# Kernel optimization log

Measured on AMD Instinct MI355X. Metric: run time of the kernel, lower is better.

Reference implementation:

```python
import jax, jax.numpy as jnp
import numpy as np

NUM_HEADS = 16
MEMORY_LR = 0.1


def setup_inputs() -> dict:
    key = jax.random.key(0)
    ks = jax.random.split(key, 5)
    B, S, D = 4, 4096, 1024
    x = jax.random.normal(ks[0], (B, S, D), dtype=jnp.float32)
    # torch init: randn * 0.01, shape (out_features, in_features)
    Wq = jax.random.normal(ks[1], (D, D), dtype=jnp.float32) * 0.01
    Wk = jax.random.normal(ks[2], (D, D), dtype=jnp.float32) * 0.01
    Wv = jax.random.normal(ks[3], (D, D), dtype=jnp.float32) * 0.01
    Wo = jax.random.normal(ks[4], (D, D), dtype=jnp.float32) * 0.01
    return {"x": x, "Wq": Wq, "Wk": Wk, "Wv": Wv, "Wo": Wo}


def reference(x, Wq, Wk, Wv, Wo):
    B, S, D = x.shape
    H = NUM_HEADS
    hd = D // H
    # Projections (torch Linear: y = x @ W^T). Pending self-mod updates
    # (immediate_update=False) never change W during forward -> plain matmul.
    Q = (x @ Wq.T).reshape(B, S, H, hd)
    K = (x @ Wk.T).reshape(B, S, H, hd)
    V = (x @ Wv.T).reshape(B, S, H, hd)
    # time-major for scan: [S, B, H, hd]
    Qt = jnp.transpose(Q, (1, 0, 2, 3))
    Kt = jnp.transpose(K, (1, 0, 2, 3))
    Vt = jnp.transpose(V, (1, 0, 2, 3))

    def step(M, qkv):
        q, k, v = qkv  # each [B, H, hd]
        v_pred = jnp.einsum('hdk,bhk->bhd', M, k)
        err = v - v_pred
        # torch computes the update under no_grad -> constant w.r.t. params
        upd = jax.lax.stop_gradient(jnp.einsum('bhd,bhk->hdk', err, k) / B)
        M_new = M + MEMORY_LR * upd
        out = jnp.einsum('hdk,bhk->bhd', M_new, q)
        return M_new, out

    M0 = jnp.zeros((H, hd, hd), dtype=x.dtype)  # memory buffer starts at zero
    _, outs = jax.lax.scan(step, M0, (Qt, Kt, Vt))  # outs: [S, B, H, hd]
    out = jnp.transpose(outs, (1, 0, 2, 3)).reshape(B, S, D)
    # dropout p=0.0 -> identity
    return out @ Wo.T
```

## Files before the change

### kernel.cpp

```cpp
#include <hip/hip_runtime.h>


typedef unsigned short u16;
typedef __attribute__((ext_vector_type(8))) short short8;
typedef __attribute__((ext_vector_type(4))) float f32x4;

#define B_ 4
#define S_ 4096
#define D_ 1024
#define H_ 16
#define CHUNK 16
#define NCHUNK 256
#define SUPW 16
#define NSUP 16
#define ETA 0.025f

__device__ __forceinline__ u16 f2bf(float f) {
  unsigned u = __builtin_bit_cast(unsigned, f);
  u += 0x7fffu + ((u >> 16) & 1u);
  return (u16)(u >> 16);
}
__device__ __forceinline__ float bf2f(u16 s) {
  unsigned u = ((unsigned)s) << 16;
  return __builtin_bit_cast(float, u);
}
__device__ __forceinline__ float ldv(float v) { return v; }
__device__ __forceinline__ float ldv(u16 v) { return bf2f(v); }
__device__ __forceinline__ void stv(float* p, float v) { *p = v; }
__device__ __forceinline__ void stv(u16* p, float v) { *p = f2bf(v); }

#define MFMA __builtin_amdgcn_mfma_f32_16x16x32_bf16

__device__ __forceinline__ void gload16(const void* g, void* l) {
  __builtin_amdgcn_global_load_lds(
      (__attribute__((address_space(1))) void*)g,
      (__attribute__((address_space(3))) void*)l, 16, 0, 0);
}

__global__ void cvt_hi_kernel(const float* __restrict__ x, u16* __restrict__ hi, int n4) {
  int i = blockIdx.x * blockDim.x + threadIdx.x;
  int stride = gridDim.x * blockDim.x;
  for (; i < n4; i += stride) {
    float4 v = ((const float4*)x)[i];
    ushort4 h;
    h.x = f2bf(v.x); h.y = f2bf(v.y); h.z = f2bf(v.z); h.w = f2bf(v.w);
    ((ushort4*)hi)[i] = h;
  }
}

template<int BPRE, typename OutT>
__global__ __launch_bounds__(256) void gemm_axw(
    const u16* __restrict__ Ahg, const void* __restrict__ Bhp,
    OutT* __restrict__ C, int M, int N, int K) {
  __shared__ __align__(16) u16 Ahs[2][128][32];
  __shared__ __align__(16) u16 Bhs[2][128][32];
  const int tid = threadIdx.x, w = tid >> 6, lane = tid & 63;
  const int nwg = gridDim.x * gridDim.y;
  const int orig = blockIdx.y * gridDim.x + blockIdx.x;
  const int id = ((nwg & 7) == 0) ? ((orig & 7) * (nwg >> 3) + (orig >> 3)) : orig;
  const int bm = (id % gridDim.x) * 128, bn = (id / gridDim.x) * 128;
  const int wm = (w >> 1) * 64, wn = (w & 1) * 64;
  const int fr = lane & 15, kb = lane >> 4;
  const int lrow = lane >> 2, lcol = (lane & 3) * 8;

  auto stage = [&](int buf, int k0) {
    {
      const size_t rb = (size_t)(bm + w * 32 + lrow) * K + k0 + lcol;
      gload16(Ahg + rb, &Ahs[buf][w * 32][0]);
      gload16(Ahg + rb + (size_t)16 * K, &Ahs[buf][w * 32 + 16][0]);
    }
    if constexpr (BPRE) {
      const u16* Bhg = (const u16*)Bhp;
      const size_t rb = (size_t)(bn + w * 32 + lrow) * K + k0 + lcol;
      gload16(Bhg + rb, &Bhs[buf][w * 32][0]);
      gload16(Bhg + rb + (size_t)16 * K, &Bhs[buf][w * 32 + 16][0]);
    } else {
      const float* Bm = (const float*)Bhp;
#pragma unroll
      for (int i2 = 0; i2 < 4; ++i2) {
        int e = tid + i2 * 256, r = e >> 3, sg = (e & 7) * 4;
        float4 v = *(const float4*)(&Bm[(size_t)(bn + r) * K + k0 + sg]);
        ushort4 hq;
        hq.x = f2bf(v.x); hq.y = f2bf(v.y); hq.z = f2bf(v.z); hq.w = f2bf(v.w);
        *(ushort4*)(&Bhs[buf][r][sg]) = hq;
      }
    }
  };

  f32x4 acc[4][4];
#pragma unroll
  for (int i = 0; i < 4; ++i)
#pragma unroll
    for (int j = 0; j < 4; ++j) acc[i][j] = (f32x4){0.f, 0.f, 0.f, 0.f};

  stage(0, 0);
  asm volatile("s_waitcnt vmcnt(0)" ::: "memory");
  __syncthreads();
  const int nt = K >> 5;
  int cur = 0;
  for (int t = 0; t < nt; ++t) {
    if (t + 1 < nt) stage(cur ^ 1, (t + 1) * 32);
    short8 ah[4], bh[4];
#pragma unroll
    for (int mi = 0; mi < 4; ++mi)
      ah[mi] = *(const short8*)(&Ahs[cur][wm + mi * 16 + fr][kb * 8]);
#pragma unroll
    for (int ni = 0; ni < 4; ++ni)
      bh[ni] = *(const short8*)(&Bhs[cur][wn + ni * 16 + fr][kb * 8]);
#pragma unroll
    for (int mi = 0; mi < 4; ++mi)
#pragma unroll
      for (int ni = 0; ni < 4; ++ni)
        acc[mi][ni] = MFMA(ah[mi], bh[ni], acc[mi][ni], 0, 0, 0);
    asm volatile("s_waitcnt vmcnt(0)" ::: "memory");
    __syncthreads();
    cur ^= 1;
  }
  const int fc = lane & 15, fr4 = (lane >> 4) * 4;
#pragma unroll
  for (int mi = 0; mi < 4; ++mi)
#pragma unroll
    for (int ni = 0; ni < 4; ++ni) {
      int gm = bm + wm + mi * 16 + fr4;
      int gn = bn + wn + ni * 16 + fc;
#pragma unroll
      for (int rg = 0; rg < 4; ++rg)
        stv(&C[(size_t)(gm + rg) * N + gn], acc[mi][ni][rg]);
    }
}

template<typename PT>
__global__ __launch_bounds__(256) void phase1_kernel(
    float* __restrict__ Qg, const u16* __restrict__ Kg, u16* __restrict__ Vg,
    PT* __restrict__ Pg, PT* __restrict__ Rg) {
  __shared__ __align__(16) u16 Ks[64][72];
  __shared__ __align__(16) u16 KsT[64][72];
  __shared__ __align__(16) u16 Gh[64][72];
  __shared__ __align__(16) u16 Gl[64][72];
  __shared__ __align__(16) float Ut[64][68];
  __shared__ __align__(16) float Wt[64][68];

  const int c = blockIdx.x, h = blockIdx.y, tid = threadIdx.x;
  const int w = tid >> 6, lane = tid & 63;
  const int fr = lane & 15, kq = lane >> 4, orow = kq * 4;
  const int xr = 16 * w + fr;

  auto gidx = [&](int r, int d) -> size_t {
    return ((size_t)(r & 3) * S_ + (size_t)c * CHUNK + (r >> 2)) * D_ + h * 64 + d;
  };
  auto ldb = [&](const u16 (*M)[72], int row, int s) -> short8 {
    return *(const short8*)(&M[row][32 * s + 8 * kq]);
  };
  auto ldm = [&](const u16 (*M)[72], int row, int s, bool up) -> short8 {
    short8 r = *(const short8*)(&M[row][32 * s + 8 * kq]);
    int rb = row >> 2, k0 = 32 * s + 8 * kq;
#pragma unroll
    for (int j = 0; j < 8; ++j) {
      int kb2 = (k0 + j) >> 2;
      bool keep = up ? (kb2 > rb) : (rb > kb2);
      if (!keep) r[j] = 0;
    }
    return r;
  };
  auto ldf = [&](const float (*M)[68], int row, int s, short8& hh, short8& ll) {
    const float* p = &M[row][32 * s + 8 * kq];
#pragma unroll
    for (int j = 0; j < 8; ++j) {
      float v = p[j];
      u16 hb = f2bf(v);
      hh[j] = (short)hb;
      ll[j] = (short)f2bf(v - bf2f(hb));
    }
  };
  auto ldfh = [&](const float (*M)[68], int row, int s) -> short8 {
    const float* p = &M[row][32 * s + 8 * kq];
    short8 hh;
#pragma unroll
    for (int j = 0; j < 8; ++j) hh[j] = (short)f2bf(p[j]);
    return hh;
  };

  for (int i = tid; i < 4096; i += 256) {
    int r = i >> 6, d = i & 63;
    size_t g = gidx(r, d);
    u16 kraw = Kg[g];
    Ks[r][d] = kraw;
    KsT[d][r] = kraw;
    Wt[d][r] = ETA * bf2f(kraw);
    Ut[d][r] = ETA * bf2f(Vg[g]);
  }
  __syncthreads();

  {
    f32x4 acc[4];
#pragma unroll
    for (int ni = 0; ni < 4; ++ni) acc[ni] = (f32x4){0.f, 0.f, 0.f, 0.f};
    short8 xf[2];
#pragma unroll
    for (int s = 0; s < 2; ++s) xf[s] = ldb(Ks, xr, s);
#pragma unroll
    for (int ni = 0; ni < 4; ++ni)
#pragma unroll
      for (int s = 0; s < 2; ++s)
        acc[ni] = MFMA(xf[s], ldb(Ks, 16 * ni + fr, s), acc[ni], 0, 0, 0);
#pragma unroll
    for (int ni = 0; ni < 4; ++ni)
#pragma unroll
      for (int rg = 0; rg < 4; ++rg) {
        float v = -ETA * acc[ni][rg];
        u16 hb = f2bf(v);
        int rr = 16 * w + orow + rg, cc = 16 * ni + fr;
        Gh[rr][cc] = hb;
        Gl[rr][cc] = f2bf(v - bf2f(hb));
      }
  }

  float sreg[4][4];
  {
    short8 xh[2], xl[2];
#pragma unroll
    for (int s = 0; s < 2; ++s) {
      const float* qp = &Qg[gidx(xr, 32 * s + 8 * kq)];
#pragma unroll
      for (int j = 0; j < 8; ++j) {
        float v = qp[j];
        u16 hb = f2bf(v);
        xh[s][j] = (short)hb;
        xl[s][j] = (short)f2bf(v - bf2f(hb));
      }
    }
    f32x4 acc[4];
#pragma unroll
    for (int ni = 0; ni < 4; ++ni) acc[ni] = (f32x4){0.f, 0.f, 0.f, 0.f};
#pragma unroll
    for (int ni = 0; ni < 4; ++ni)
#pragma unroll
      for (int s = 0; s < 2; ++s) {
        short8 yf = ldb(Ks, 16 * ni + fr, s);
        acc[ni] = MFMA(xh[s], yf, acc[ni], 0, 0, 0);
        acc[ni] = MFMA(xl[s], yf, acc[ni], 0, 0, 0);
      }
#pragma unroll
    for (int ni = 0; ni < 4; ++ni)
#pragma unroll
      for (int rg = 0; rg < 4; ++rg) {
        int r = 16 * w + orow + rg, cc = 16 * ni + fr;
        sreg[ni][rg] = ((r >> 2) >= (cc >> 2)) ? acc[ni][rg] : 0.f;
      }
  }
  __syncthreads();

  auto app1 = [&](float (*St)[68]) {
    short8 xh[2], xl[2];
#pragma unroll
    for (int s = 0; s < 2; ++s) ldf(St, xr, s, xh[s], xl[s]);
    f32x4 acc[4];
#pragma unroll
    for (int ni = 0; ni < 4; ++ni) acc[ni] = (f32x4){0.f, 0.f, 0.f, 0.f};
#pragma unroll
    for (int ni = 0; ni < 4; ++ni)
#pragma unroll
      for (int s = 0; s < 2; ++s) {
        short8 yh = ldm(Gh, 16 * ni + fr, s, false);
        short8 yl = ldm(Gl, 16 * ni + fr, s, false);
        acc[ni] = MFMA(xh[s], yh, acc[ni], 0, 0, 0);
        acc[ni] = MFMA(xh[s], yl, acc[ni], 0, 0, 0);
        acc[ni] = MFMA(xl[s], yh, acc[ni], 0, 0, 0);
      }
#pragma unroll
    for (int ni = 0; ni < 4; ++ni)
#pragma unroll
      for (int rg = 0; rg < 4; ++rg)
        St[16 * w + orow + rg][16 * ni + fr] += acc[ni][rg];
  };
  auto appS = [&](float (*St)[68], const u16 (*Np)[72]) {
    short8 xh[2];
#pragma unroll
    for (int s = 0; s < 2; ++s) xh[s] = ldfh(St, xr, s);
    f32x4 acc[4];
#pragma unroll
    for (int ni = 0; ni < 4; ++ni) acc[ni] = (f32x4){0.f, 0.f, 0.f, 0.f};
#pragma unroll
    for (int ni = 0; ni < 4; ++ni)
#pragma unroll
      for (int s = 0; s < 2; ++s)
        acc[ni] = MFMA(xh[s], ldb(Np, 16 * ni + fr, s), acc[ni], 0, 0, 0);
#pragma unroll
    for (int ni = 0; ni < 4; ++ni)
#pragma unroll
      for (int rg = 0; rg < 4; ++rg)
        St[16 * w + orow + rg][16 * ni + fr] += acc[ni][rg];
  };

  app1(Ut);
  app1(Wt);
  {
    f32x4 sq[4];
#pragma unroll
    for (int ni = 0; ni < 4; ++ni) sq[ni] = (f32x4){0.f, 0.f, 0.f, 0.f};
    short8 xh[2], xl[2];
#pragma unroll
    for (int s = 0; s < 2; ++s) {
      xh[s] = ldm(Gh, xr, s, false);
      xl[s] = ldm(Gl, xr, s, false);
    }
#pragma unroll
    for (int ni = 0; ni < 4; ++ni)
#pragma unroll
      for (int s = 0; s < 2; ++s) {
        short8 yh = ldm(Gh, 16 * ni + fr, s, true);
        short8 yl = ldm(Gl, 16 * ni + fr, s, true);
        sq[ni] = MFMA(xh[s], yh, sq[ni], 0, 0, 0);
        sq[ni] = MFMA(xh[s], yl, sq[ni], 0, 0, 0);
        sq[ni] = MFMA(xl[s], yh, sq[ni], 0, 0, 0);
      }
    __syncthreads();
#pragma unroll
    for (int ni = 0; ni < 4; ++ni)
#pragma unroll
      for (int rg = 0; rg < 4; ++rg) {
        u16 b = f2bf(sq[ni][rg]);
        int rr = 16 * w + orow + rg, cc = 16 * ni + fr;
        Ks[rr][cc] = b;
        Gh[cc][rr] = b;
      }
  }
  __syncthreads();

  appS(Ut, Ks);
  appS(Wt, Ks);
  {
    f32x4 sq[4];
#pragma unroll
    for (int ni = 0; ni < 4; ++ni) sq[ni] = (f32x4){0.f, 0.f, 0.f, 0.f};
    short8 xf[2];
#pragma unroll
    for (int s = 0; s < 2; ++s) xf[s] = ldb(Ks, xr, s);
#pragma unroll
    for (int ni = 0; ni < 4; ++ni)
#pragma unroll
      for (int s = 0; s < 2; ++s)
        sq[ni] = MFMA(xf[s], ldb(Gh, 16 * ni + fr, s), sq[ni], 0, 0, 0);
    __syncthreads();
#pragma unroll
    for (int ni = 0; ni < 4; ++ni)
#pragma unroll
      for (int rg = 0; rg < 4; ++rg) {
        u16 b = f2bf(sq[ni][rg]);
        int rr = 16 * w + orow + rg, cc = 16 * ni + fr;
        Gl[rr][cc] = b;
        Ks[cc][rr] = b;
      }
  }
  __syncthreads();

  appS(Ut, Gl);
  appS(Wt, Gl);
  {
    f32x4 sq[4];
#pragma unroll
    for (int ni = 0; ni < 4; ++ni) sq[ni] = (f32x4){0.f, 0.f, 0.f, 0.f};
    short8 xf[2];
#pragma unroll
    for (int s = 0; s < 2; ++s) xf[s] = ldb(Gl, xr, s);
#pragma unroll
    for (int ni = 0; ni < 4; ++ni)
#pragma unroll
      for (int s = 0; s < 2; ++s)
        sq[ni] = MFMA(xf[s], ldb(Ks, 16 * ni + fr, s), sq[ni], 0, 0, 0);
#pragma unroll
    for (int ni = 0; ni < 4; ++ni)
#pragma unroll
      for (int rg = 0; rg < 4; ++rg)
        Gh[16 * w + orow + rg][16 * ni + fr] = f2bf(sq[ni][rg]);
  }
  __syncthreads();

  appS(Ut, Gh);
  appS(Wt, Gh);
  __syncthreads();

  const size_t base = ((size_t)c * H_ + h) * 4096;
  {
    short8 xh[2], xl[2];
#pragma unroll
    for (int s = 0; s < 2; ++s) ldf(Wt, xr, s, xh[s], xl[s]);
    f32x4 acc[4];
#pragma unroll
    for (int ni = 0; ni < 4; ++ni) acc[ni] = (f32x4){0.f, 0.f, 0.f, 0.f};
#pragma unroll
    for (int ni = 0; ni < 4; ++ni)
#pragma unroll
      for (int s = 0; s < 2; ++s) {
        short8 yf = ldb(KsT, 16 * ni + fr, s);
        acc[ni] = MFMA(xh[s], yf, acc[ni], 0, 0, 0);
        acc[ni] = MFMA(xl[s], yf, acc[ni], 0, 0, 0);
      }
#pragma unroll
    for (int ni = 0; ni < 4; ++ni)
#pragma unroll
      for (int rg = 0; rg < 4; ++rg)
        stv(&Pg[base + (16 * w + orow + rg) * 64 + 16 * ni + fr], acc[ni][rg]);
  }
  {
    short8 xh[2], xl[2];
#pragma unroll
    for (int s = 0; s < 2; ++s) ldf(Ut, xr, s, xh[s], xl[s]);
    f32x4 acc[4];
#pragma unroll
    for (int ni = 0; ni < 4; ++ni) acc[ni] = (f32x4){0.f, 0.f, 0.f, 0.f};
#pragma unroll
    for (int ni = 0; ni < 4; ++ni)
#pragma unroll
      for (int s = 0; s < 2; ++s) {
        short8 yf = ldb(KsT, 16 * ni + fr, s);
        acc[ni] = MFMA(xh[s], yf, acc[ni], 0, 0, 0);
        acc[ni] = MFMA(xl[s], yf, acc[ni], 0, 0, 0);
      }
#pragma unroll
    for (int ni = 0; ni < 4; ++ni)
#pragma unroll
      for (int rg = 0; rg < 4; ++rg)
        stv(&Rg[base + (16 * w + orow + rg) * 64 + 16 * ni + fr], acc[ni][rg]);
  }
  {
    const int r = tid >> 2, d0 = (tid & 3) * 16;
    short8 v0, v1;
#pragma unroll
    for (int j = 0; j < 8; ++j) v0[j] = (short)f2bf(Wt[r][d0 + j]);
#pragma unroll
    for (int j = 0; j < 8; ++j) v1[j] = (short)f2bf(Wt[r][d0 + 8 + j]);
    *(short8*)(&Gh[r][d0]) = v0;
    *(short8*)(&Gh[r][d0 + 8]) = v1;
#pragma unroll
    for (int j = 0; j < 8; ++j) v0[j] = (short)f2bf(Ut[r][d0 + j]);
#pragma unroll
    for (int j = 0; j < 8; ++j) v1[j] = (short)f2bf(Ut[r][d0 + 8 + j]);
    *(short8*)(&Gl[r][d0]) = v0;
    *(short8*)(&Gl[r][d0 + 8]) = v1;
  }
#pragma unroll
  for (int ni = 0; ni < 4; ++ni)
#pragma unroll
    for (int rg = 0; rg < 4; ++rg)
      Ks[16 * w + orow + rg][16 * ni + fr] = f2bf(sreg[ni][rg]);
  __syncthreads();

  {
    short8 xs[2];
#pragma unroll
    for (int s = 0; s < 2; ++s) xs[s] = ldb(Ks, xr, s);
    f32x4 accE[4], accF[4];
#pragma unroll
    for (int ni = 0; ni < 4; ++ni) {
      accE[ni] = (f32x4){0.f, 0.f, 0.f, 0.f};
      accF[ni] = (f32x4){0.f, 0.f, 0.f, 0.f};
    }
#pragma unroll
    for (int ni = 0; ni < 4; ++ni)
#pragma unroll
      for (int s = 0; s < 2; ++s) {
        accE[ni] = MFMA(xs[s], ldb(Gh, 16 * ni + fr, s), accE[ni], 0, 0, 0);
        accF[ni] = MFMA(xs[s], ldb(Gl, 16 * ni + fr, s), accF[ni], 0, 0, 0);
      }
#pragma unroll
    for (int ni = 0; ni < 4; ++ni)
#pragma unroll
      for (int rg = 0; rg < 4; ++rg) {
        int r = 16 * w + orow + rg, d = 16 * ni + fr;
        size_t g = gidx(r, d);
        float qv = Qg[g];
        Qg[g] = qv - accE[ni][rg];
        Vg[g] = f2bf(accF[ni][rg]);
      }
  }
}

__device__ __forceinline__ void store64(float* dst, const float (*src)[65], int tid) {
  for (int i = tid; i < 4096; i += 256) dst[i] = src[i >> 6][i & 63];
}
__device__ __forceinline__ void mm64(const float (*X)[65], const float (*Y)[65],
                                     float (*Dst)[65], const float (*Add)[65], int tid) {
  const int r0 = (tid >> 4) * 4, c0 = (tid & 15) * 4;
  float a[4][4] = {};
  for (int d = 0; d < 64; ++d) {
    float xv[4], yv[4];
#pragma unroll
    for (int i = 0; i < 4; ++i) xv[i] = X[r0 + i][d];
#pragma unroll
    for (int j = 0; j < 4; ++j) yv[j] = Y[d][c0 + j];
#pragma unroll
    for (int i = 0; i < 4; ++i)
#pragma unroll
      for (int j = 0; j < 4; ++j) a[i][j] += xv[i] * yv[j];
  }
  __syncthreads();
#pragma unroll
  for (int i = 0; i < 4; ++i)
#pragma unroll
    for (int j = 0; j < 4; ++j) {
      float v = a[i][j];
      if (Add) v += Add[r0 + i][c0 + j];
      Dst[r0 + i][c0 + j] = v;
    }
  __syncthreads();
}

template<typename PT>
__global__ __launch_bounds__(256) void seq_levelA(const PT* __restrict__ Pg,
    const PT* __restrict__ Rg, float* __restrict__ Psup, float* __restrict__ Rsup) {
  __shared__ __align__(16) float Pa[64][68], Ra[64][68], Ri[64][68];
  __shared__ __align__(16) u16 Pih[64][72], Pil[64][72];
  const int sup = blockIdx.x, h = blockIdx.y, tid = threadIdx.x;
  const int w = tid >> 6, lane = tid & 63;
  const int fr = lane & 15, kq = lane >> 4, orow = kq * 4;
  const int xr = 16 * w + fr;
  const int cbase = sup * SUPW;

  auto upd = [&](float (*St)[68], const float (*Add)[68]) {
    short8 xh[2], xl[2];
#pragma unroll
    for (int s2 = 0; s2 < 2; ++s2) {
      const float* p = &St[xr][32 * s2 + 8 * kq];
#pragma unroll
      for (int j = 0; j < 8; ++j) {
        float v = p[j];
        u16 hb = f2bf(v);
        xh[s2][j] = (short)hb;
        xl[s2][j] = (short)f2bf(v - bf2f(hb));
      }
    }
    f32x4 acc[4];
#pragma unroll
    for (int ni = 0; ni < 4; ++ni) acc[ni] = (f32x4){0.f, 0.f, 0.f, 0.f};
#pragma unroll
    for (int ni = 0; ni < 4; ++ni)
#pragma unroll
      for (int s2 = 0; s2 < 2; ++s2) {
        short8 yh = *(const short8*)(&Pih[16 * ni + fr][32 * s2 + 8 * kq]);
        short8 yl = *(const short8*)(&Pil[16 * ni + fr][32 * s2 + 8 * kq]);
        acc[ni] = MFMA(xh[s2], yh, acc[ni], 0, 0, 0);
        acc[ni] = MFMA(xh[s2], yl, acc[ni], 0, 0, 0);
        acc[ni] = MFMA(xl[s2], yh, acc[ni], 0, 0, 0);
      }
#pragma unroll
    for (int ni = 0; ni < 4; ++ni)
#pragma unroll
      for (int rg = 0; rg < 4; ++rg) {
        float v = acc[ni][rg];
        if (Add) v += Add[16 * w + orow + rg][16 * ni + fr];
        St[16 * w + orow + rg][16 * ni + fr] = v;
      }
  };

  {
    const PT* ps = Pg + ((size_t)cbase * H_ + h) * 4096;
    const PT* rs = Rg + ((size_t)cbase * H_ + h) * 4096;
    for (int i = tid; i < 4096; i += 256) {
      int r = i >> 6, cc = i & 63;
      Pa[r][cc] = ((r == cc) ? 1.f : 0.f) - ldv(ps[i]);
      Ra[r][cc] = ldv(rs[i]);
    }
  }
  float pf[16], rf[16];
  {
    const PT* ps = Pg + ((size_t)(cbase + 1) * H_ + h) * 4096;
    const PT* rs = Rg + ((size_t)(cbase + 1) * H_ + h) * 4096;
#pragma unroll
    for (int k = 0; k < 16; ++k) { int i = tid + k * 256; pf[k] = ldv(ps[i]); rf[k] = ldv(rs[i]); }
  }
  for (int s = 1; s < SUPW; ++s) {
#pragma unroll
    for (int k = 0; k < 16; ++k) {
      int i = tid + k * 256, d = i >> 6, cc = i & 63;
      float v = ((d == cc) ? 1.f : 0.f) - pf[k];
      u16 hb = f2bf(v);
      Pih[cc][d] = hb;
      Pil[cc][d] = f2bf(v - bf2f(hb));
      Ri[d][cc] = rf[k];
    }
    __syncthreads();
    if (s + 1 < SUPW) {
      const PT* ps = Pg + ((size_t)(cbase + s + 1) * H_ + h) * 4096;
      const PT* rs = Rg + ((size_t)(cbase + s + 1) * H_ + h) * 4096;
#pragma unroll
      for (int k = 0; k < 16; ++k) { int i = tid + k * 256; pf[k] = ldv(ps[i]); rf[k] = ldv(rs[i]); }
    }
    upd(Pa, nullptr);
    upd(Ra, Ri);
    __syncthreads();
  }
  for (int i = tid; i < 4096; i += 256) {
    Psup[((size_t)sup * H_ + h) * 4096 + i] = Pa[i >> 6][i & 63];
    Rsup[((size_t)sup * H_ + h) * 4096 + i] = Ra[i >> 6][i & 63];
  }
}

__global__ __launch_bounds__(256) void seq_levelB(const float* __restrict__ Psup,
    const float* __restrict__ Rsup, float* __restrict__ Msup) {
  __shared__ float Ms[64][65], Pi[64][65], Ri[64][65];
  const int h = blockIdx.x, tid = threadIdx.x;
  for (int i = tid; i < 4096; i += 256) Ms[i >> 6][i & 63] = 0.f;
  float pf[16], rf[16];
  {
    const float* ps = Psup + ((size_t)0 * H_ + h) * 4096;
    const float* rs = Rsup + ((size_t)0 * H_ + h) * 4096;
#pragma unroll
    for (int k = 0; k < 16; ++k) { int i = tid + k * 256; pf[k] = ps[i]; rf[k] = rs[i]; }
  }
  for (int s = 0; s < NSUP; ++s) {
#pragma unroll
    for (int k = 0; k < 16; ++k) {
      int i = tid + k * 256, r = i >> 6, cc = i & 63;
      Pi[r][cc] = pf[k];
      Ri[r][cc] = rf[k];
    }
    store64(Msup + ((size_t)s * H_ + h) * 4096, Ms, tid);
    __syncthreads();
    if (s + 1 < NSUP) {
      const float* ps = Psup + ((size_t)(s + 1) * H_ + h) * 4096;
      const float* rs = Rsup + ((size_t)(s + 1) * H_ + h) * 4096;
#pragma unroll
      for (int k = 0; k < 16; ++k) { int i = tid + k * 256; pf[k] = ps[i]; rf[k] = rs[i]; }
    }
    mm64(Ms, Pi, Ms, Ri, tid);
  }
}

template<typename PT>
__global__ __launch_bounds__(256) void seq_levelC(const PT* __restrict__ Pg,
    PT* __restrict__ Rg, const float* __restrict__ Msup) {
  __shared__ __align__(16) float Ms[64][68], Ri[64][68];
  __shared__ __align__(16) u16 Pih[64][72], Pil[64][72];
  const int sup = blockIdx.x, h = blockIdx.y, tid = threadIdx.x;
  const int w = tid >> 6, lane = tid & 63;
  const int fr = lane & 15, kq = lane >> 4, orow = kq * 4;
  const int xr = 16 * w + fr;

  auto upd = [&](float (*St)[68], const float (*Add)[68]) {
    short8 xh[2], xl[2];
#pragma unroll
    for (int s2 = 0; s2 < 2; ++s2) {
      const float* p = &St[xr][32 * s2 + 8 * kq];
#pragma unroll
      for (int j = 0; j < 8; ++j) {
        float v = p[j];
        u16 hb = f2bf(v);
        xh[s2][j] = (short)hb;
        xl[s2][j] = (short)f2bf(v - bf2f(hb));
      }
    }
    f32x4 acc[4];
#pragma unroll
    for (int ni = 0; ni < 4; ++ni) acc[ni] = (f32x4){0.f, 0.f, 0.f, 0.f};
#pragma unroll
    for (int ni = 0; ni < 4; ++ni)
#pragma unroll
      for (int s2 = 0; s2 < 2; ++s2) {
        short8 yh = *(const short8*)(&Pih[16 * ni + fr][32 * s2 + 8 * kq]);
        short8 yl = *(const short8*)(&Pil[16 * ni + fr][32 * s2 + 8 * kq]);
        acc[ni] = MFMA(xh[s2], yh, acc[ni], 0, 0, 0);
        acc[ni] = MFMA(xh[s2], yl, acc[ni], 0, 0, 0);
        acc[ni] = MFMA(xl[s2], yh, acc[ni], 0, 0, 0);
      }
#pragma unroll
    for (int ni = 0; ni < 4; ++ni)
#pragma unroll
      for (int rg = 0; rg < 4; ++rg) {
        float v = acc[ni][rg];
        if (Add) v += Add[16 * w + orow + rg][16 * ni + fr];
        St[16 * w + orow + rg][16 * ni + fr] = v;
      }
  };

  for (int i = tid; i < 4096; i += 256)
    Ms[i >> 6][i & 63] = Msup[((size_t)sup * H_ + h) * 4096 + i];
  float pf[16], rf[16];
  {
    const size_t slice = ((size_t)(sup * SUPW) * H_ + h) * 4096;
#pragma unroll
    for (int k = 0; k < 16; ++k) { int i = tid + k * 256; pf[k] = ldv(Pg[slice + i]); rf[k] = ldv(Rg[slice + i]); }
  }
  for (int s = 0; s < SUPW; ++s) {
    const size_t slice = ((size_t)(sup * SUPW + s) * H_ + h) * 4096;
#pragma unroll
    for (int k = 0; k < 16; ++k) {
      int i = tid + k * 256, d = i >> 6, cc = i & 63;
      float v = ((d == cc) ? 1.f : 0.f) - pf[k];
      u16 hb = f2bf(v);
      Pih[cc][d] = hb;
      Pil[cc][d] = f2bf(v - bf2f(hb));
      Ri[d][cc] = rf[k];
    }
    for (int i = tid; i < 4096; i += 256) stv(&Rg[slice + i], Ms[i >> 6][i & 63]);
    __syncthreads();
    if (s + 1 < SUPW) {
      const size_t sl2 = ((size_t)(sup * SUPW + s + 1) * H_ + h) * 4096;
#pragma unroll
      for (int k = 0; k < 16; ++k) { int i = tid + k * 256; pf[k] = ldv(Pg[sl2 + i]); rf[k] = ldv(Rg[sl2 + i]); }
    }
    upd(Ms, Ri);
    __syncthreads();
  }
}

template<typename PT>
__global__ __launch_bounds__(256) void phase3_kernel(
    const float* __restrict__ Eg, const u16* __restrict__ Fg,
    const PT* __restrict__ Mcg, u16* __restrict__ attn) {
  __shared__ float Es[64][65], Ms[64][65];
  const int c = blockIdx.x, h = blockIdx.y, tid = threadIdx.x;
  for (int i = tid; i < 4096; i += 256) {
    int r = i >> 6, d = i & 63, t = r >> 2, b = r & 3;
    size_t g = ((size_t)b * S_ + (size_t)c * CHUNK + t) * D_ + h * 64 + d;
    Es[r][d] = Eg[g];
    Ms[i >> 6][i & 63] = ldv(Mcg[((size_t)c * H_ + h) * 4096 + i]);
  }
  __syncthreads();
  const int r0 = (tid >> 4) * 4, d0 = (tid & 15) * 4;
  float a[4][4] = {};
  for (int k = 0; k < 64; ++k) {
    float ev[4], mv[4];
#pragma unroll
    for (int i = 0; i < 4; ++i) ev[i] = Es[r0 + i][k];
#pragma unroll
    for (int j = 0; j < 4; ++j) mv[j] = Ms[d0 + j][k];
#pragma unroll
    for (int i = 0; i < 4; ++i)
#pragma unroll
      for (int j = 0; j < 4; ++j) a[i][j] += ev[i] * mv[j];
  }
#pragma unroll
  for (int i = 0; i < 4; ++i)
#pragma unroll
    for (int j = 0; j < 4; ++j) {
      int r = r0 + i, d = d0 + j, t = r >> 2, b = r & 3;
      size_t g = ((size_t)b * S_ + (size_t)c * CHUNK + t) * D_ + h * 64 + d;
      attn[g] = f2bf(a[i][j] + bf2f(Fg[g]));
    }
}

extern "C" void kernel_launch(void* const* d_in, const int* in_sizes, int n_in,
                              void* d_out, int out_size, void* d_ws, size_t ws_size,
                              hipStream_t stream) {
  (void)in_sizes; (void)n_in; (void)out_size;
  const float* x  = (const float*)d_in[0];
  const float* Wq = (const float*)d_in[1];
  const float* Wk = (const float*)d_in[2];
  const float* Wv = (const float*)d_in[3];
  const float* Wo = (const float*)d_in[4];
  float* out = (float*)d_out;

  char* w = (char*)d_ws;
  const size_t MB = 1024 * 1024;
  u16* Kbf = (u16*)w;
  u16* Vbf = (u16*)(w + 32 * MB);
  u16* xh  = (u16*)(w + 64 * MB);
  const bool big = ws_size >= 192 * MB;
  void* Preg = (void*)(w + 64 * MB);
  void* Rreg = big ? (void*)(w + 128 * MB) : (void*)(w + 96 * MB);
  float* Psup = (float*)w;
  float* Rsup = (float*)(w + 4 * MB);
  float* Msup = (float*)(w + 8 * MB);
  u16* attn = (u16*)Preg;
  u16* Wsp = (u16*)(w + 128 * MB);

  const size_t DSZ = (size_t)B_ * S_ * D_;
  cvt_hi_kernel<<<2048, 256, 0, stream>>>(x, xh, (int)(DSZ / 4));

  dim3 gg(128, 8);
  if (big) {
    cvt_hi_kernel<<<512, 256, 0, stream>>>(Wq, Wsp + 0 * 1048576u, 262144);
    cvt_hi_kernel<<<512, 256, 0, stream>>>(Wk, Wsp + 1 * 1048576u, 262144);
    cvt_hi_kernel<<<512, 256, 0, stream>>>(Wv, Wsp + 2 * 1048576u, 262144);
    gemm_axw<1, float><<<gg, 256, 0, stream>>>(xh, Wsp + 0 * 1048576u, out, 16384, 1024, 1024);
    gemm_axw<1, u16><<<gg, 256, 0, stream>>>(xh, Wsp + 1 * 1048576u, Kbf, 16384, 1024, 1024);
    gemm_axw<1, u16><<<gg, 256, 0, stream>>>(xh, Wsp + 2 * 1048576u, Vbf, 16384, 1024, 1024);
    float* P = (float*)Preg; float* R = (float*)Rreg;
    phase1_kernel<float><<<dim3(NCHUNK, H_), 256, 0, stream>>>(out, Kbf, Vbf, P, R);
    seq_levelA<float><<<dim3(NSUP, H_), 256, 0, stream>>>(P, R, Psup, Rsup);
    seq_levelB<<<dim3(H_), 256, 0, stream>>>(Psup, Rsup, Msup);
    seq_levelC<float><<<dim3(NSUP, H_), 256, 0, stream>>>(P, R, Msup);
    phase3_kernel<float><<<dim3(NCHUNK, H_), 256, 0, stream>>>(out, Vbf, R, attn);
    cvt_hi_kernel<<<512, 256, 0, stream>>>(Wo, Wsp + 0 * 1048576u, 262144);
    gemm_axw<1, float><<<gg, 256, 0, stream>>>(attn, Wsp + 0 * 1048576u, out, 16384, 1024, 1024);
  } else {
    gemm_axw<0, float><<<gg, 256, 0, stream>>>(xh, Wq, out, 16384, 1024, 1024);
    gemm_axw<0, u16><<<gg, 256, 0, stream>>>(xh, Wk, Kbf, 16384, 1024, 1024);
    gemm_axw<0, u16><<<gg, 256, 0, stream>>>(xh, Wv, Vbf, 16384, 1024, 1024);
    u16* P = (u16*)Preg; u16* R = (u16*)Rreg;
    phase1_kernel<u16><<<dim3(NCHUNK, H_), 256, 0, stream>>>(out, Kbf, Vbf, P, R);
    seq_levelA<u16><<<dim3(NSUP, H_), 256, 0, stream>>>(P, R, Psup, Rsup);
    seq_levelB<<<dim3(H_), 256, 0, stream>>>(Psup, Rsup, Msup);
    seq_levelC<u16><<<dim3(NSUP, H_), 256, 0, stream>>>(P, R, Msup);
    phase3_kernel<u16><<<dim3(NCHUNK, H_), 256, 0, stream>>>(out, Vbf, R, attn);
    gemm_axw<0, float><<<gg, 256, 0, stream>>>(attn, Wo, out, 16384, 1024, 1024);
  }
}
```

Before: 581.2 us.

## Triple-buffer bf16 GEMM loads and fuse paired phase1 MFMA chains with premasked operands

For GEMMs whose B operand is already bf16, the loop now keeps three LDS buffers with two stages in flight. It waits with a partial vmcnt and one barrier per iteration instead of fully draining each step. In phase1 the strictly-lower mask is applied once when the G matrix is written, with transposed copies kept in new LDS arrays, so per-load masking (ldm) is removed. The paired U/W updates and the P/R output matmuls are merged into single loops to raise MFMA interleaving, at the cost of more LDS and registers.

```diff
diff --git a/kernel.cpp b/kernel.cpp
--- a/kernel.cpp
+++ b/kernel.cpp
@@ -52,8 +52,9 @@
 __global__ __launch_bounds__(256) void gemm_axw(
     const u16* __restrict__ Ahg, const void* __restrict__ Bhp,
     OutT* __restrict__ C, int M, int N, int K) {
-  __shared__ __align__(16) u16 Ahs[2][128][32];
-  __shared__ __align__(16) u16 Bhs[2][128][32];
+  constexpr int NB = BPRE ? 3 : 2;
+  __shared__ __align__(16) u16 Ahs[NB][128][32];
+  __shared__ __align__(16) u16 Bhs[NB][128][32];
   const int tid = threadIdx.x, w = tid >> 6, lane = tid & 63;
   const int nwg = gridDim.x * gridDim.y;
   const int orig = blockIdx.y * gridDim.x + blockIdx.x;
@@ -86,35 +87,51 @@
       }
     }
   };
-
-  f32x4 acc[4][4];
-#pragma unroll
-  for (int i = 0; i < 4; ++i)
-#pragma unroll
-    for (int j = 0; j < 4; ++j) acc[i][j] = (f32x4){0.f, 0.f, 0.f, 0.f};
-
-  stage(0, 0);
-  asm volatile("s_waitcnt vmcnt(0)" ::: "memory");
-  __syncthreads();
-  const int nt = K >> 5;
-  int cur = 0;
-  for (int t = 0; t < nt; ++t) {
-    if (t + 1 < nt) stage(cur ^ 1, (t + 1) * 32);
+  auto compute = [&](int buf, f32x4 (*acc)[4]) {
     short8 ah[4], bh[4];
 #pragma unroll
     for (int mi = 0; mi < 4; ++mi)
-      ah[mi] = *(const short8*)(&Ahs[cur][wm + mi * 16 + fr][kb * 8]);
-#pragma unroll
-    for (int ni = 0; ni < 4; ++ni)
-      bh[ni] = *(const short8*)(&Bhs[cur][wn + ni * 16 + fr][kb * 8]);
+      ah[mi] = *(const short8*)(&Ahs[buf][wm + mi * 16 + fr][kb * 8]);
+#pragma unroll
+    for (int ni = 0; ni < 4; ++ni)
+      bh[ni] = *(const short8*)(&Bhs[buf][wn + ni * 16 + fr][kb * 8]);
 #pragma unroll
     for (int mi = 0; mi < 4; ++mi)
 #pragma unroll
       for (int ni = 0; ni < 4; ++ni)
         acc[mi][ni] = MFMA(ah[mi], bh[ni], acc[mi][ni], 0, 0, 0);
+  };
+
+  f32x4 acc[4][4];
+#pragma unroll
+  for (int i = 0; i < 4; ++i)
+#pragma unroll
+    for (int j = 0; j < 4; ++j) acc[i][j] = (f32x4){0.f, 0.f, 0.f, 0.f};
+
+  const int nt = K >> 5;
+  if constexpr (BPRE) {
+    stage(0, 0);
+    stage(1, 32);
+    for (int t = 0; t < nt; ++t) {
+      if (t + 1 < nt) asm volatile("s_waitcnt vmcnt(4)" ::: "memory");
+      else            asm volatile("s_waitcnt vmcnt(0)" ::: "memory");
+      __builtin_amdgcn_s_barrier();
+      __builtin_amdgcn_sched_barrier(0);
+      if (t + 2 < nt) stage((t + 2) % 3, (t + 2) * 32);
+      compute(t % 3, acc);
+    }
+  } else {
+    stage(0, 0);
     asm volatile("s_waitcnt vmcnt(0)" ::: "memory");
     __syncthreads();
-    cur ^= 1;
+    int cur = 0;
+    for (int t = 0; t < nt; ++t) {
+      if (t + 1 < nt) stage(cur ^ 1, (t + 1) * 32);
+      compute(cur, acc);
+      asm volatile("s_waitcnt vmcnt(0)" ::: "memory");
+      __syncthreads();
+      cur ^= 1;
+    }
   }
   const int fc = lane & 15, fr4 = (lane >> 4) * 4;
 #pragma unroll
@@ -137,6 +154,7 @@
   __shared__ __align__(16) u16 KsT[64][72];
   __shared__ __align__(16) u16 Gh[64][72];
   __shared__ __align__(16) u16 Gl[64][72];
+  __shared__ __align__(16) u16 Xs[64][72];
   __shared__ __align__(16) float Ut[64][68];
   __shared__ __align__(16) float Wt[64][68];
 
@@ -150,17 +168,6 @@
   };
   auto ldb = [&](const u16 (*M)[72], int row, int s) -> short8 {
     return *(const short8*)(&M[row][32 * s + 8 * kq]);
-  };
-  auto ldm = [&](const u16 (*M)[72], int row, int s, bool up) -> short8 {
-    short8 r = *(const short8*)(&M[row][32 * s + 8 * kq]);
-    int rb = row >> 2, k0 = 32 * s + 8 * kq;
-#pragma unroll
-    for (int j = 0; j < 8; ++j) {
-      int kb2 = (k0 + j) >> 2;
-      bool keep = up ? (kb2 > rb) : (rb > kb2);
-      if (!keep) r[j] = 0;
-    }
-    return r;
   };
   auto ldf = [&](const float (*M)[68], int row, int s, short8& hh, short8& ll) {
     const float* p = &M[row][32 * s + 8 * kq];
@@ -191,10 +198,10 @@
   }
   __syncthreads();
 
-  {
-    f32x4 acc[4];
-#pragma unroll
-    for (int ni = 0; ni < 4; ++ni) acc[ni] = (f32x4){0.f, 0.f, 0.f, 0.f};
+  f32x4 gacc[4];
+#pragma unroll
+  for (int ni = 0; ni < 4; ++ni) gacc[ni] = (f32x4){0.f, 0.f, 0.f, 0.f};
+  {
     short8 xf[2];
 #pragma unroll
     for (int s = 0; s < 2; ++s) xf[s] = ldb(Ks, xr, s);
@@ -202,17 +209,7 @@
     for (int ni = 0; ni < 4; ++ni)
 #pragma unroll
       for (int s = 0; s < 2; ++s)
-        acc[ni] = MFMA(xf[s], ldb(Ks, 16 * ni + fr, s), acc[ni], 0, 0, 0);
-#pragma unroll
-    for (int ni = 0; ni < 4; ++ni)
-#pragma unroll
-      for (int rg = 0; rg < 4; ++rg) {
-        float v = -ETA * acc[ni][rg];
-        u16 hb = f2bf(v);
-        int rr = 16 * w + orow + rg, cc = 16 * ni + fr;
-        Gh[rr][cc] = hb;
-        Gl[rr][cc] = f2bf(v - bf2f(hb));
-      }
+        gacc[ni] = MFMA(xf[s], ldb(Ks, 16 * ni + fr, s), gacc[ni], 0, 0, 0);
   }
 
   float sreg[4][4];
@@ -250,66 +247,88 @@
   }
   __syncthreads();
 
-  auto app1 = [&](float (*St)[68]) {
-    short8 xh[2], xl[2];
-#pragma unroll
-    for (int s = 0; s < 2; ++s) ldf(St, xr, s, xh[s], xl[s]);
-    f32x4 acc[4];
-#pragma unroll
-    for (int ni = 0; ni < 4; ++ni) acc[ni] = (f32x4){0.f, 0.f, 0.f, 0.f};
+#pragma unroll
+  for (int ni = 0; ni < 4; ++ni)
+#pragma unroll
+    for (int rg = 0; rg < 4; ++rg) {
+      float v = -ETA * gacc[ni][rg];
+      u16 hb = f2bf(v);
+      u16 lb = f2bf(v - bf2f(hb));
+      int rr = 16 * w + orow + rg, cc = 16 * ni + fr;
+      bool low = (rr >> 2) > (cc >> 2);
+      u16 hm = low ? hb : (u16)0, lm = low ? lb : (u16)0;
+      Gh[rr][cc] = hm;
+      Gl[rr][cc] = lm;
+      Ks[cc][rr] = hm;
+      Xs[cc][rr] = lm;
+    }
+  __syncthreads();
+
+  {
+    short8 uh[2], ul[2], wh[2], wl[2];
+#pragma unroll
+    for (int s = 0; s < 2; ++s) { ldf(Ut, xr, s, uh[s], ul[s]); ldf(Wt, xr, s, wh[s], wl[s]); }
+    f32x4 aU[4], aW[4];
+#pragma unroll
+    for (int ni = 0; ni < 4; ++ni) { aU[ni] = (f32x4){0.f,0.f,0.f,0.f}; aW[ni] = (f32x4){0.f,0.f,0.f,0.f}; }
 #pragma unroll
     for (int ni = 0; ni < 4; ++ni)
 #pragma unroll
       for (int s = 0; s < 2; ++s) {
-        short8 yh = ldm(Gh, 16 * ni + fr, s, false);
-        short8 yl = ldm(Gl, 16 * ni + fr, s, false);
-        acc[ni] = MFMA(xh[s], yh, acc[ni], 0, 0, 0);
-        acc[ni] = MFMA(xh[s], yl, acc[ni], 0, 0, 0);
-        acc[ni] = MFMA(xl[s], yh, acc[ni], 0, 0, 0);
-      }
-#pragma unroll
-    for (int ni = 0; ni < 4; ++ni)
-#pragma unroll
-      for (int rg = 0; rg < 4; ++rg)
-        St[16 * w + orow + rg][16 * ni + fr] += acc[ni][rg];
-  };
-  auto appS = [&](float (*St)[68], const u16 (*Np)[72]) {
-    short8 xh[2];
-#pragma unroll
-    for (int s = 0; s < 2; ++s) xh[s] = ldfh(St, xr, s);
-    f32x4 acc[4];
-#pragma unroll
-    for (int ni = 0; ni < 4; ++ni) acc[ni] = (f32x4){0.f, 0.f, 0.f, 0.f};
-#pragma unroll
-    for (int ni = 0; ni < 4; ++ni)
-#pragma unroll
-      for (int s = 0; s < 2; ++s)
-        acc[ni] = MFMA(xh[s], ldb(Np, 16 * ni + fr, s), acc[ni], 0, 0, 0);
-#pragma unroll
-    for (int ni = 0; ni < 4; ++ni)
-#pragma unroll
-      for (int rg = 0; rg < 4; ++rg)
-        St[16 * w + orow + rg][16 * ni + fr] += acc[ni][rg];
-  };
-
-  app1(Ut);
-  app1(Wt);
+        short8 yh = ldb(Gh, 16 * ni + fr, s);
+        short8 yl = ldb(Gl, 16 * ni + fr, s);
+        aU[ni] = MFMA(uh[s], yh, aU[ni], 0, 0, 0);
+        aU[ni] = MFMA(uh[s], yl, aU[ni], 0, 0, 0);
+        aU[ni] = MFMA(ul[s], yh, aU[ni], 0, 0, 0);
+        aW[ni] = MFMA(wh[s], yh, aW[ni], 0, 0, 0);
+        aW[ni] = MFMA(wh[s], yl, aW[ni], 0, 0, 0);
+        aW[ni] = MFMA(wl[s], yh, aW[ni], 0, 0, 0);
+      }
+#pragma unroll
+    for (int ni = 0; ni < 4; ++ni)
+#pragma unroll
+      for (int rg = 0; rg < 4; ++rg) {
+        Ut[16 * w + orow + rg][16 * ni + fr] += aU[ni][rg];
+        Wt[16 * w + orow + rg][16 * ni + fr] += aW[ni][rg];
+      }
+  }
+  auto appSf = [&](const u16 (*Np)[72]) {
+    short8 xu[2], xw[2];
+#pragma unroll
+    for (int s = 0; s < 2; ++s) { xu[s] = ldfh(Ut, xr, s); xw[s] = ldfh(Wt, xr, s); }
+    f32x4 aU[4], aW[4];
+#pragma unroll
+    for (int ni = 0; ni < 4; ++ni) { aU[ni] = (f32x4){0.f,0.f,0.f,0.f}; aW[ni] = (f32x4){0.f,0.f,0.f,0.f}; }
+#pragma unroll
+    for (int ni = 0; ni < 4; ++ni)
+#pragma unroll
+      for (int s = 0; s < 2; ++s) {
+        short8 yf = ldb(Np, 16 * ni + fr, s);
+        aU[ni] = MFMA(xu[s], yf, aU[ni], 0, 0, 0);
+        aW[ni] = MFMA(xw[s], yf, aW[ni], 0, 0, 0);
+      }
+#pragma unroll
+    for (int ni = 0; ni < 4; ++ni)
+#pragma unroll
+      for (int rg = 0; rg < 4; ++rg) {
+        Ut[16 * w + orow + rg][16 * ni + fr] += aU[ni][rg];
+        Wt[16 * w + orow + rg][16 * ni + fr] += aW[ni][rg];
+      }
+  };
+
   {
     f32x4 sq[4];
 #pragma unroll
     for (int ni = 0; ni < 4; ++ni) sq[ni] = (f32x4){0.f, 0.f, 0.f, 0.f};
     short8 xh[2], xl[2];
 #pragma unroll
-    for (int s = 0; s < 2; ++s) {
-      xh[s] = ldm(Gh, xr, s, false);
-      xl[s] = ldm(Gl, xr, s, false);
-    }
+    for (int s = 0; s < 2; ++s) { xh[s] = ldb(Gh, xr, s); xl[s] = ldb(Gl, xr, s); }
 #pragma unroll
     for (int ni = 0; ni < 4; ++ni)
 #pragma unroll
       for (int s = 0; s < 2; ++s) {
-        short8 yh = ldm(Gh, 16 * ni + fr, s, true);
-        short8 yl = ldm(Gl, 16 * ni + fr, s, true);
+        short8 yh = ldb(Ks, 16 * ni + fr, s);
+        short8 yl = ldb(Xs, 16 * ni + fr, s);
         sq[ni] = MFMA(xh[s], yh, sq[ni], 0, 0, 0);
         sq[ni] = MFMA(xh[s], yl, sq[ni], 0, 0, 0);
         sq[ni] = MFMA(xl[s], yh, sq[ni], 0, 0, 0);
@@ -327,8 +346,7 @@
   }
   __syncthreads();
 
-  appS(Ut, Ks);
-  appS(Wt, Ks);
+  appSf(Ks);
   {
     f32x4 sq[4];
 #pragma unroll
@@ -354,8 +372,7 @@
   }
   __syncthreads();
 
-  appS(Ut, Gl);
-  appS(Wt, Gl);
+  appSf(Gl);
   {
     f32x4 sq[4];
 #pragma unroll
@@ -376,52 +393,34 @@
   }
   __syncthreads();
 
-  appS(Ut, Gh);
-  appS(Wt, Gh);
+  appSf(Gh);
   __syncthreads();
 
   const size_t base = ((size_t)c * H_ + h) * 4096;
   {
-    short8 xh[2], xl[2];
-#pragma unroll
-    for (int s = 0; s < 2; ++s) ldf(Wt, xr, s, xh[s], xl[s]);
-    f32x4 acc[4];
-#pragma unroll
-    for (int ni = 0; ni < 4; ++ni) acc[ni] = (f32x4){0.f, 0.f, 0.f, 0.f};
+    short8 wh[2], wl[2], uh[2], ul[2];
+#pragma unroll
+    for (int s = 0; s < 2; ++s) { ldf(Wt, xr, s, wh[s], wl[s]); ldf(Ut, xr, s, uh[s], ul[s]); }
+    f32x4 aP[4], aR[4];
+#pragma unroll
+    for (int ni = 0; ni < 4; ++ni) { aP[ni] = (f32x4){0.f,0.f,0.f,0.f}; aR[ni] = (f32x4){0.f,0.f,0.f,0.f}; }
 #pragma unroll
     for (int ni = 0; ni < 4; ++ni)
 #pragma unroll
       for (int s = 0; s < 2; ++s) {
         short8 yf = ldb(KsT, 16 * ni + fr, s);
-        acc[ni] = MFMA(xh[s], yf, acc[ni], 0, 0, 0);
-        acc[ni] = MFMA(xl[s], yf, acc[ni], 0, 0, 0);
-      }
-#pragma unroll
-    for (int ni = 0; ni < 4; ++ni)
-#pragma unroll
-      for (int rg = 0; rg < 4; ++rg)
-        stv(&Pg[base + (16 * w + orow + rg) * 64 + 16 * ni + fr], acc[ni][rg]);
-  }
-  {
-    short8 xh[2], xl[2];
-#pragma unroll
-    for (int s = 0; s < 2; ++s) ldf(Ut, xr, s, xh[s], xl[s]);
-    f32x4 acc[4];
-#pragma unroll
-    for (int ni = 0; ni < 4; ++ni) acc[ni] = (f32x4){0.f, 0.f, 0.f, 0.f};
-#pragma unroll
-    for (int ni = 0; ni < 4; ++ni)
-#pragma unroll
-      for (int s = 0; s < 2; ++s) {
-        short8 yf = ldb(KsT, 16 * ni + fr, s);
-        acc[ni] = MFMA(xh[s], yf, acc[ni], 0, 0, 0);
-        acc[ni] = MFMA(xl[s], yf, acc[ni], 0, 0, 0);
-      }
-#pragma unroll
-    for (int ni = 0; ni < 4; ++ni)
-#pragma unroll
-      for (int rg = 0; rg < 4; ++rg)
-        stv(&Rg[base + (16 * w + orow + rg) * 64 + 16 * ni + fr], acc[ni][rg]);
+        aP[ni] = MFMA(wh[s], yf, aP[ni], 0, 0, 0);
+        aP[ni] = MFMA(wl[s], yf, aP[ni], 0, 0, 0);
+        aR[ni] = MFMA(uh[s], yf, aR[ni], 0, 0, 0);
+        aR[ni] = MFMA(ul[s], yf, aR[ni], 0, 0, 0);
+      }
+#pragma unroll
+    for (int ni = 0; ni < 4; ++ni)
+#pragma unroll
+      for (int rg = 0; rg < 4; ++rg) {
+        stv(&Pg[base + (16 * w + orow + rg) * 64 + 16 * ni + fr], aP[ni][rg]);
+        stv(&Rg[base + (16 * w + orow + rg) * 64 + 16 * ni + fr], aR[ni][rg]);
+      }
   }
   {
     const int r = tid >> 2, d0 = (tid & 3) * 16;
```

Measured after the change: 604.2 us. 1.04x slower.
